# Kernel tuning notes

Hardware: AMD Instinct MI355X
Metric: run time of the kernel (lower is better)

## Reference

```python
import jax, jax.numpy as jnp
import numpy as np

H = 128   # LSTM hidden size
T = 120   # sequence length
F = 4     # input features


def setup_inputs() -> dict:
    key = jax.random.key(0)
    ks = jax.random.split(key, 11)
    B = 4096
    return {
        "x": jax.random.normal(ks[0], (B, T, F), dtype=jnp.float32),
        "h0": jax.random.uniform(ks[1], (B, H), dtype=jnp.float32),
        "c0": jax.random.uniform(ks[2], (B, H), dtype=jnp.float32),
        "W_ih": jax.random.normal(ks[3], (4 * H, F), dtype=jnp.float32) * 0.05,
        "W_hh": jax.random.normal(ks[4], (4 * H, H), dtype=jnp.float32) * 0.05,
        "b_ih": jax.random.normal(ks[5], (4 * H,), dtype=jnp.float32) * 0.05,
        "b_hh": jax.random.normal(ks[6], (4 * H,), dtype=jnp.float32) * 0.05,
        "fc1_w": jax.random.normal(ks[7], (100, T * H), dtype=jnp.float32) * 0.01,
        "fc1_b": jax.random.normal(ks[8], (100,), dtype=jnp.float32) * 0.01,
        "fc2_w": jax.random.normal(ks[9], (10, 100), dtype=jnp.float32) * 0.1,
        "fc2_b": jax.random.normal(ks[10], (10,), dtype=jnp.float32) * 0.1,
    }


def _lstm(x, h0, c0, W_ih, W_hh, b_ih, b_hh):
    # Precompute input-dependent part of the gates for all timesteps at once.
    # PyTorch gate order: i, f, g, o.  gates_x: [T, B, 4H]
    gates_x = jnp.einsum('btf,gf->tbg', x, W_ih) + b_ih + b_hh

    def step(carry, gx):
        h, c = carry
        g = gx + h @ W_hh.T                      # [B, 4H]
        i = jax.nn.sigmoid(g[:, 0 * H:1 * H])
        f = jax.nn.sigmoid(g[:, 1 * H:2 * H])
        gg = jnp.tanh(g[:, 2 * H:3 * H])
        o = jax.nn.sigmoid(g[:, 3 * H:4 * H])
        c = f * c + i * gg
        h = o * jnp.tanh(c)
        return (h, c), h

    (_, _), hs = jax.lax.scan(step, (h0, c0), gates_x)  # hs: [T, B, H]
    return hs


def reference(x, h0, c0, W_ih, W_hh, b_ih, b_hh, fc1_w, fc1_b, fc2_w, fc2_b):
    B = x.shape[0]
    hs = _lstm(x, h0, c0, W_ih, W_hh, b_ih, b_hh)        # [T, B, H]
    feat = hs.transpose(1, 0, 2).reshape(B, T * H)        # [B, T*H]
    hid = jax.nn.relu(feat @ fc1_w.T + fc1_b)             # [B, 100]
    logits = hid @ fc2_w.T + fc2_b                        # [B, 10]
    return jax.nn.log_softmax(logits, axis=-1)
```

## Files before the change

### kernel.cpp

```cpp
#include <hip/hip_runtime.h>

#define T_LEN 120
#define H 128
#define ROWS 16
#define FC1_STRIDE 15360

#define OFF_WHH   0u
#define OFF_WXB   131072u
#define OFF_FC1W  163840u
#define OFF_FC1B  4096000u

typedef short short8 __attribute__((ext_vector_type(8)));
typedef float f32x4 __attribute__((ext_vector_type(4)));
typedef unsigned int ui32x4 __attribute__((ext_vector_type(4)));

#define L2E 1.4426950408889634f
#define SWZ(r) (((((r) & 7) ^ (((r) >> 3) << 1))) << 4)
#define MFMA __builtin_amdgcn_mfma_f32_16x16x32_bf16
#define BAR() do { asm volatile("s_waitcnt lgkmcnt(0)" ::: "memory"); \
                   __builtin_amdgcn_s_barrier(); \
                   asm volatile("" ::: "memory"); } while (0)

__device__ __forceinline__ unsigned short f2bu(float f) {
  unsigned u = __builtin_bit_cast(unsigned, f);
  u += 0x7fffu + ((u >> 16) & 1u);
  return (unsigned short)(u >> 16);
}
__device__ __forceinline__ float gate_scale(int row) {
  return ((row >> 7) == 2) ? 2.0f * L2E : -L2E;
}

__global__ void prep_all(const float* __restrict__ W_ih, const float* __restrict__ W_hh,
                         const float* __restrict__ b_ih, const float* __restrict__ b_hh,
                         const float* __restrict__ fc1_w, const float* __restrict__ fc1_b,
                         unsigned char* __restrict__ ws) {
  if (blockIdx.x < 1024) {
    unsigned short* w = (unsigned short*)(ws + OFF_FC1W);
    int j = blockIdx.x >> 3;
    int c0 = ((blockIdx.x & 7) * 256 + threadIdx.x) * 8;
    if (c0 >= FC1_STRIDE) return;
    short8 v = {0, 0, 0, 0, 0, 0, 0, 0};
    if (j < 100) {
      const float* src = fc1_w + j * FC1_STRIDE + c0;
#pragma unroll
      for (int e = 0; e < 8; ++e) ((unsigned short*)&v)[e] = f2bu(src[e]);
    }
    *(short8*)(w + j * FC1_STRIDE + c0) = v;
  } else {
    unsigned short* whh = (unsigned short*)(ws + OFF_WHH);
    unsigned short* wxb = (unsigned short*)(ws + OFF_WXB);
    float* fb = (float*)(ws + OFF_FC1B);
    int tid = (blockIdx.x - 1024) * 256 + threadIdx.x;
    const int nt = 8 * 256;
    for (int i = tid; i < 512 * 128; i += nt) {
      int row = i >> 7;
      whh[i] = f2bu(W_hh[i] * gate_scale(row));
    }
    for (int i = tid; i < 512 * 32; i += nt) {
      int j = i >> 5, k = i & 31;
      float s = gate_scale(j);
      float v = 0.f;
      if (k < 4) v = W_ih[j * 4 + k] * s;
      else if (k == 4) v = (b_ih[j] + b_hh[j]) * s;
      wxb[i] = f2bu(v);
    }
    for (int i = tid; i < 128; i += nt) fb[i] = (i < 100) ? fc1_b[i] : 0.f;
  }
}

__global__ __launch_bounds__(512, 2)
void lstm_fused(const float* __restrict__ x, const float* __restrict__ h0,
                const float* __restrict__ c0, const float* __restrict__ fc2_w,
                const float* __restrict__ fc2_b, const unsigned char* __restrict__ ws,
                float* __restrict__ out) {
  __shared__ __align__(16) unsigned char xab[T_LEN * 256];
  __shared__ __align__(16) unsigned char h_lds[2 * 4096];
  __shared__ __align__(16) float fc2w_s[1000];
  __shared__ float fc2b_s[10];
  __shared__ float logit_s[ROWS * 12];

  const int tid = threadIdx.x;
  const int w = tid >> 6;
  const int l = tid & 63;
  const int lq = l >> 4;
  const int lc = l & 15;
  const int r0 = blockIdx.x * ROWS;
  const int hcol = w * 16 + lc;

  const unsigned short* Whh = (const unsigned short*)(ws + OFF_WHH);
  const unsigned short* Wxb = (const unsigned short*)(ws + OFF_WXB);
  const unsigned short* FC1 = (const unsigned short*)(ws + OFF_FC1W);
  const float* FC1B = (const float*)(ws + OFF_FC1B);

  for (int i = tid; i < 1000; i += 512) fc2w_s[i] = fc2_w[i];
  if (tid < 10) fc2b_s[tid] = fc2_b[tid];

  for (int i = tid; i < ROWS * T_LEN; i += 512) {
    int rr = i / T_LEN, t = i - rr * T_LEN;
    f32x4 xv = *(const f32x4*)(x + (r0 + rr) * (T_LEN * 4) + t * 4);
    unsigned w0 = (unsigned)f2bu(xv[0]) | ((unsigned)f2bu(xv[1]) << 16);
    unsigned w1 = (unsigned)f2bu(xv[2]) | ((unsigned)f2bu(xv[3]) << 16);
    ui32x4 pk = {w0, w1, 0x3f80u, 0u};
    *(ui32x4*)(xab + t * 256 + rr * 16) = pk;
  }
  for (int e = tid * 2; e < ROWS * H; e += 1024) {
    int r = e >> 7, c = e & 127;
    unsigned u = (unsigned)f2bu(h0[(r0 + r) * H + c]) |
                 ((unsigned)f2bu(h0[(r0 + r) * H + c + 1]) << 16);
    *(unsigned*)(h_lds + 4096 + r * 256 + ((2 * c) ^ SWZ(r))) = u;
  }
  float c_reg[4];
#pragma unroll
  for (int q = 0; q < 4; ++q) c_reg[q] = c0[(r0 + lq * 4 + q) * H + hcol];

  short8 bhh[4][4], bxb[4];
#pragma unroll
  for (int g = 0; g < 4; ++g) {
    int n0 = (g * 8 + w) * 16;
#pragma unroll
    for (int kk = 0; kk < 4; ++kk)
      bhh[g][kk] = *(const short8*)(Whh + (n0 + lc) * H + kk * 32 + lq * 8);
    bxb[g] = *(const short8*)(Wxb + (n0 + lc) * 32 + lq * 8);
  }
  const unsigned short* fc1row = FC1 + (w * 16 + lc) * FC1_STRIDE;
  f32x4 facc = {0.f, 0.f, 0.f, 0.f};

  __syncthreads();

  short8 ha[4];
#pragma unroll
  for (int kk = 0; kk < 4; ++kk)
    ha[kk] = *(const short8*)(h_lds + 4096 + lc * 256 + ((kk * 64 + lq * 16) ^ SWZ(lc)));
  short8 xa = *(const short8*)(xab + lc * 16);

  const f32x4 zero4 = {0.f, 0.f, 0.f, 0.f};
  f32x4 accX0 = MFMA(xa, bxb[0], zero4, 0, 0, 0);
  f32x4 accX1 = MFMA(xa, bxb[1], zero4, 0, 0, 0);
  f32x4 accX2 = MFMA(xa, bxb[2], zero4, 0, 0, 0);
  f32x4 accX3 = MFMA(xa, bxb[3], zero4, 0, 0, 0);

  for (int t = 0; t < T_LEN; ++t) {
    __builtin_amdgcn_s_setprio(1);
    f32x4 acc0 = accX0, acc1 = accX1, acc2 = accX2, acc3 = accX3;
#pragma unroll
    for (int kk = 0; kk < 4; ++kk) {
      acc0 = MFMA(ha[kk], bhh[0][kk], acc0, 0, 0, 0);
      acc1 = MFMA(ha[kk], bhh[1][kk], acc1, 0, 0, 0);
      acc2 = MFMA(ha[kk], bhh[2][kk], acc2, 0, 0, 0);
      acc3 = MFMA(ha[kk], bhh[3][kk], acc3, 0, 0, 0);
    }

    const unsigned short* fp = fc1row + t * 128 + lq * 8;
    short8 fb0 = *(const short8*)(fp + 0);
    short8 fb1 = *(const short8*)(fp + 32);
    short8 fb2 = *(const short8*)(fp + 64);
    short8 fb3 = *(const short8*)(fp + 96);
    int tn = (t + 1 < T_LEN) ? t + 1 : t;
    short8 xan = *(const short8*)(xab + tn * 256 + lc * 16);

    unsigned char* hw = h_lds + (t & 1) * 4096;
#pragma unroll
    for (int qp = 0; qp < 2; ++qp) {
      const int q0 = qp * 2, q1 = q0 + 1;
      float ea0 = __builtin_amdgcn_exp2f(acc0[q0]), ea1 = __builtin_amdgcn_exp2f(acc0[q1]);
      float eb0 = __builtin_amdgcn_exp2f(acc1[q0]), eb1 = __builtin_amdgcn_exp2f(acc1[q1]);
      float ec0 = __builtin_amdgcn_exp2f(acc2[q0]), ec1 = __builtin_amdgcn_exp2f(acc2[q1]);
      float ed0 = __builtin_amdgcn_exp2f(acc3[q0]), ed1 = __builtin_amdgcn_exp2f(acc3[q1]);
      float a0 = 1.f + ea0, b0 = 1.f + eb0, d0 = 1.f + ec0, e0 = 1.f + ed0;
      float a1 = 1.f + ea1, b1 = 1.f + eb1, d1 = 1.f + ec1, e1 = 1.f + ed1;
      float ab0 = a0 * b0, ab1 = a1 * b1, de0 = d0 * e0, de1 = d1 * e1;
      float rAB = __builtin_amdgcn_rcpf(ab0 * ab1);
      float rDE = __builtin_amdgcn_rcpf(de0 * de1);
      float rab0 = rAB * ab1, rab1 = rAB * ab0;
      float rde0 = rDE * de1, rde1 = rDE * de0;
      float iv0 = b0 * rab0, fv0 = a0 * rab0;
      float iv1 = b1 * rab1, fv1 = a1 * rab1;
      float gv0 = 1.f - 2.f * (e0 * rde0), ov0 = d0 * rde0;
      float gv1 = 1.f - 2.f * (e1 * rde1), ov1 = d1 * rde1;
      float cn0 = fv0 * c_reg[q0] + iv0 * gv0;
      float cn1 = fv1 * c_reg[q1] + iv1 * gv1;
      c_reg[q0] = cn0; c_reg[q1] = cn1;
      float et0 = __builtin_amdgcn_exp2f(2.8853900817779268f * cn0);
      float et1 = __builtin_amdgcn_exp2f(2.8853900817779268f * cn1);
      float t0 = 1.f + et0, t1 = 1.f + et1;
      float rT = __builtin_amdgcn_rcpf(t0 * t1);
      float hv0 = ov0 * (1.f - 2.f * (rT * t1));
      float hv1 = ov1 * (1.f - 2.f * (rT * t0));
      int r0r = lq * 4 + q0, r1r = lq * 4 + q1;
      *(unsigned short*)(hw + r0r * 256 + ((2 * hcol) ^ SWZ(r0r))) = f2bu(hv0);
      *(unsigned short*)(hw + r1r * 256 + ((2 * hcol) ^ SWZ(r1r))) = f2bu(hv1);
    }
    __builtin_amdgcn_s_setprio(0);

    accX0 = MFMA(xan, bxb[0], zero4, 0, 0, 0);
    accX1 = MFMA(xan, bxb[1], zero4, 0, 0, 0);
    accX2 = MFMA(xan, bxb[2], zero4, 0, 0, 0);
    accX3 = MFMA(xan, bxb[3], zero4, 0, 0, 0);

    BAR();

#pragma unroll
    for (int kk = 0; kk < 4; ++kk)
      ha[kk] = *(const short8*)(hw + lc * 256 + ((kk * 64 + lq * 16) ^ SWZ(lc)));
    facc = MFMA(ha[0], fb0, facc, 0, 0, 0);
    facc = MFMA(ha[1], fb1, facc, 0, 0, 0);
    facc = MFMA(ha[2], fb2, facc, 0, 0, 0);
    facc = MFMA(ha[3], fb3, facc, 0, 0, 0);
  }

  float bias = FC1B[hcol];
  __syncthreads();
  float* hid = (float*)xab;
#pragma unroll
  for (int q = 0; q < 4; ++q) {
    float v = facc[q] + bias;
    hid[(lq * 4 + q) * 132 + hcol] = v > 0.f ? v : 0.f;
  }
  __syncthreads();
  if (tid < 160) {
    int r = tid & 15, k = tid >> 4;
    float a = fc2b_s[k];
#pragma unroll 4
    for (int j = 0; j < 100; ++j) a += hid[r * 132 + j] * fc2w_s[k * 100 + j];
    logit_s[r * 12 + k] = a;
  }
  __syncthreads();
  if (tid < 16) {
    int r = tid;
    float m = logit_s[r * 12];
#pragma unroll
    for (int k = 1; k < 10; ++k) m = fmaxf(m, logit_s[r * 12 + k]);
    float s = 0.f;
#pragma unroll
    for (int k = 0; k < 10; ++k)
      s += __builtin_amdgcn_exp2f(L2E * (logit_s[r * 12 + k] - m));
    float ls = __builtin_amdgcn_logf(s) * 0.6931471805599453f;
#pragma unroll
    for (int k = 0; k < 10; ++k)
      out[(r0 + r) * 10 + k] = logit_s[r * 12 + k] - m - ls;
  }
}

extern "C" void kernel_launch(void* const* d_in, const int* in_sizes, int n_in,
                              void* d_out, int out_size, void* d_ws, size_t ws_size,
                              hipStream_t stream) {
  const float* x     = (const float*)d_in[0];
  const float* h0    = (const float*)d_in[1];
  const float* c0    = (const float*)d_in[2];
  const float* W_ih  = (const float*)d_in[3];
  const float* W_hh  = (const float*)d_in[4];
  const float* b_ih  = (const float*)d_in[5];
  const float* b_hh  = (const float*)d_in[6];
  const float* fc1_w = (const float*)d_in[7];
  const float* fc1_b = (const float*)d_in[8];
  const float* fc2_w = (const float*)d_in[9];
  const float* fc2_b = (const float*)d_in[10];
  float* out = (float*)d_out;
  unsigned char* ws = (unsigned char*)d_ws;

  prep_all<<<1032, 256, 0, stream>>>(W_ih, W_hh, b_ih, b_hh, fc1_w, fc1_b, ws);
  lstm_fused<<<256, 512, 0, stream>>>(x, h0, c0, fc2_w, fc2_b, ws, out);
}
```

Before: 147.2 us.

## Split recurrent MFMA chains, defer fc1 MFMAs, use packed bf16 conversion

Splits each gate's recurrent MFMA accumulation into two independent chains (lo/hi K halves) that are summed afterwards, shortening the dependent MFMA chain on the per-step critical path. The fc1 accumulation MFMAs are moved from after the barrier to the start of the next iteration, where they overlap with the recurrent work, and the last step is drained after the loop. Scalar bf16 rounding is replaced with the hardware v_cvt_pk_bf16_f32 instruction, and the swizzled LDS store offsets are precomputed once. The extra vector adds and the added register pressure could offset part of the latency saved.

Result: no change. 145.7 us (-1.0%).

```diff
diff --git a/kernel.cpp b/kernel.cpp
--- a/kernel.cpp
+++ b/kernel.cpp
@@ -25,6 +25,11 @@
   unsigned u = __builtin_bit_cast(unsigned, f);
   u += 0x7fffu + ((u >> 16) & 1u);
   return (unsigned short)(u >> 16);
+}
+__device__ __forceinline__ unsigned cvt_pk_bf16(float lo, float hi) {
+  unsigned r;
+  asm("v_cvt_pk_bf16_f32 %0, %1, %2" : "=v"(r) : "v"(lo), "v"(hi));
+  return r;
 }
 __device__ __forceinline__ float gate_scale(int row) {
   return ((row >> 7) == 2) ? 2.0f * L2E : -L2E;
@@ -98,8 +103,8 @@
   for (int i = tid; i < ROWS * T_LEN; i += 512) {
     int rr = i / T_LEN, t = i - rr * T_LEN;
     f32x4 xv = *(const f32x4*)(x + (r0 + rr) * (T_LEN * 4) + t * 4);
-    unsigned w0 = (unsigned)f2bu(xv[0]) | ((unsigned)f2bu(xv[1]) << 16);
-    unsigned w1 = (unsigned)f2bu(xv[2]) | ((unsigned)f2bu(xv[3]) << 16);
+    unsigned w0 = cvt_pk_bf16(xv[0], xv[1]);
+    unsigned w1 = cvt_pk_bf16(xv[2], xv[3]);
     ui32x4 pk = {w0, w1, 0x3f80u, 0u};
     *(ui32x4*)(xab + t * 256 + rr * 16) = pk;
   }
@@ -125,6 +130,13 @@
   const unsigned short* fc1row = FC1 + (w * 16 + lc) * FC1_STRIDE;
   f32x4 facc = {0.f, 0.f, 0.f, 0.f};
 
+  unsigned soff[4];
+#pragma unroll
+  for (int q = 0; q < 4; ++q) {
+    int r = lq * 4 + q;
+    soff[q] = (unsigned)(r * 256 + ((2 * hcol) ^ SWZ(r)));
+  }
+
   __syncthreads();
 
   short8 ha[4];
@@ -139,22 +151,45 @@
   f32x4 accX2 = MFMA(xa, bxb[2], zero4, 0, 0, 0);
   f32x4 accX3 = MFMA(xa, bxb[3], zero4, 0, 0, 0);
 
+  short8 fbh0 = {0,0,0,0,0,0,0,0}, fbh1 = {0,0,0,0,0,0,0,0};
+  short8 fbh2 = {0,0,0,0,0,0,0,0}, fbh3 = {0,0,0,0,0,0,0,0};
+
   for (int t = 0; t < T_LEN; ++t) {
     __builtin_amdgcn_s_setprio(1);
-    f32x4 acc0 = accX0, acc1 = accX1, acc2 = accX2, acc3 = accX3;
-#pragma unroll
-    for (int kk = 0; kk < 4; ++kk) {
-      acc0 = MFMA(ha[kk], bhh[0][kk], acc0, 0, 0, 0);
-      acc1 = MFMA(ha[kk], bhh[1][kk], acc1, 0, 0, 0);
-      acc2 = MFMA(ha[kk], bhh[2][kk], acc2, 0, 0, 0);
-      acc3 = MFMA(ha[kk], bhh[3][kk], acc3, 0, 0, 0);
-    }
+    f32x4 lo0 = accX0, lo1 = accX1, lo2 = accX2, lo3 = accX3;
+    f32x4 hi0 = zero4, hi1 = zero4, hi2 = zero4, hi3 = zero4;
+    lo0 = MFMA(ha[0], bhh[0][0], lo0, 0, 0, 0);
+    lo1 = MFMA(ha[0], bhh[1][0], lo1, 0, 0, 0);
+    lo2 = MFMA(ha[0], bhh[2][0], lo2, 0, 0, 0);
+    lo3 = MFMA(ha[0], bhh[3][0], lo3, 0, 0, 0);
+    hi0 = MFMA(ha[2], bhh[0][2], hi0, 0, 0, 0);
+    hi1 = MFMA(ha[2], bhh[1][2], hi1, 0, 0, 0);
+    hi2 = MFMA(ha[2], bhh[2][2], hi2, 0, 0, 0);
+    hi3 = MFMA(ha[2], bhh[3][2], hi3, 0, 0, 0);
+    lo0 = MFMA(ha[1], bhh[0][1], lo0, 0, 0, 0);
+    lo1 = MFMA(ha[1], bhh[1][1], lo1, 0, 0, 0);
+    lo2 = MFMA(ha[1], bhh[2][1], lo2, 0, 0, 0);
+    lo3 = MFMA(ha[1], bhh[3][1], lo3, 0, 0, 0);
+    hi0 = MFMA(ha[3], bhh[0][3], hi0, 0, 0, 0);
+    hi1 = MFMA(ha[3], bhh[1][3], hi1, 0, 0, 0);
+    hi2 = MFMA(ha[3], bhh[2][3], hi2, 0, 0, 0);
+    hi3 = MFMA(ha[3], bhh[3][3], hi3, 0, 0, 0);
+
+    facc = MFMA(ha[0], fbh0, facc, 0, 0, 0);
+    facc = MFMA(ha[1], fbh1, facc, 0, 0, 0);
+    facc = MFMA(ha[2], fbh2, facc, 0, 0, 0);
+    facc = MFMA(ha[3], fbh3, facc, 0, 0, 0);
+
+    f32x4 acc0 = lo0 + hi0;
+    f32x4 acc1 = lo1 + hi1;
+    f32x4 acc2 = lo2 + hi2;
+    f32x4 acc3 = lo3 + hi3;
 
     const unsigned short* fp = fc1row + t * 128 + lq * 8;
-    short8 fb0 = *(const short8*)(fp + 0);
-    short8 fb1 = *(const short8*)(fp + 32);
-    short8 fb2 = *(const short8*)(fp + 64);
-    short8 fb3 = *(const short8*)(fp + 96);
+    fbh0 = *(const short8*)(fp + 0);
+    fbh1 = *(const short8*)(fp + 32);
+    fbh2 = *(const short8*)(fp + 64);
+    fbh3 = *(const short8*)(fp + 96);
     int tn = (t + 1 < T_LEN) ? t + 1 : t;
     short8 xan = *(const short8*)(xab + tn * 256 + lc * 16);
 
@@ -186,9 +221,9 @@
       float rT = __builtin_amdgcn_rcpf(t0 * t1);
       float hv0 = ov0 * (1.f - 2.f * (rT * t1));
       float hv1 = ov1 * (1.f - 2.f * (rT * t0));
-      int r0r = lq * 4 + q0, r1r = lq * 4 + q1;
-      *(unsigned short*)(hw + r0r * 256 + ((2 * hcol) ^ SWZ(r0r))) = f2bu(hv0);
-      *(unsigned short*)(hw + r1r * 256 + ((2 * hcol) ^ SWZ(r1r))) = f2bu(hv1);
+      unsigned pk = cvt_pk_bf16(hv0, hv1);
+      *(unsigned short*)(hw + soff[q0]) = (unsigned short)pk;
+      *(unsigned short*)(hw + soff[q1]) = (unsigned short)(pk >> 16);
     }
     __builtin_amdgcn_s_setprio(0);
 
@@ -202,11 +237,11 @@
 #pragma unroll
     for (int kk = 0; kk < 4; ++kk)
       ha[kk] = *(const short8*)(hw + lc * 256 + ((kk * 64 + lq * 16) ^ SWZ(lc)));
-    facc = MFMA(ha[0], fb0, facc, 0, 0, 0);
-    facc = MFMA(ha[1], fb1, facc, 0, 0, 0);
-    facc = MFMA(ha[2], fb2, facc, 0, 0, 0);
-    facc = MFMA(ha[3], fb3, facc, 0, 0, 0);
-  }
+  }
+  facc = MFMA(ha[0], fbh0, facc, 0, 0, 0);
+  facc = MFMA(ha[1], fbh1, facc, 0, 0, 0);
+  facc = MFMA(ha[2], fbh2, facc, 0, 0, 0);
+  facc = MFMA(ha[3], fbh3, facc, 0, 0, 0);
 
   float bias = FC1B[hcol];
   __syncthreads();
```
